# Performance work log

Hardware: AMD Instinct MI355X
Metric: run time of the kernel (lower is better)

## Reference

```python
import jax, jax.numpy as jnp
import numpy as np

NUM_TOKEN = 1024
IN_DIM = 512
OUT_DIM = 512
E = 1024          # expansion_factor * in_token_dims
S = 128
EPS = 1e-5
SQRT_S = float(np.sqrt(S))


def _rope_seq(x):
    """RoPE over axis 1 (sequence), last axis is feature dim. x: [B, L, ..., D]."""
    L = x.shape[1]
    half = x.shape[-1] // 2
    pos = jnp.arange(L, dtype=jnp.float32)
    inv_freq = 10000.0 ** (jnp.arange(half, dtype=jnp.float32) / half)
    sinusoid = pos[:, None] * inv_freq[None, :]          # [L, half]
    bshape = (1, L) + (1,) * (x.ndim - 3) + (half,)
    sin = jnp.sin(sinusoid).reshape(bshape)
    cos = jnp.cos(sinusoid).reshape(bshape)
    x1, x2 = jnp.split(x, 2, axis=-1)
    return jnp.concatenate([x1 * cos - x2 * sin, x2 * cos + x1 * sin], axis=-1)


def setup_inputs() -> dict:
    key = jax.random.key(0)
    ks = jax.random.split(key, 8)
    B = 32
    x = jax.random.normal(ks[0], (B, NUM_TOKEN, IN_DIM), jnp.float32)
    uv_w = jax.random.normal(ks[1], (2 * E + S, IN_DIM), jnp.float32) / np.sqrt(IN_DIM)
    o_w = jax.random.normal(ks[2], (OUT_DIM, E), jnp.float32) / np.sqrt(E)
    gamma = jax.random.uniform(ks[3], (2, S), jnp.float32)
    beta = jax.random.uniform(ks[4], (2, S), jnp.float32)
    w = jax.random.uniform(ks[5], (2 * NUM_TOKEN - 1,), jnp.float32)
    g = jnp.ones((1,), jnp.float32)                       # ScaleNorm gain
    res_scale = jnp.ones((IN_DIM,), jnp.float32)
    layer_scale = jnp.ones((OUT_DIM,), jnp.float32)
    return dict(x=x, uv_w=uv_w, o_w=o_w, gamma=gamma, beta=beta, w=w,
                g=g, res_scale=res_scale, layer_scale=layer_scale)


def reference(x, uv_w, o_w, gamma, beta, w, g, res_scale, layer_scale):
    B, L, D = x.shape
    # ScaleNorm
    norm = jnp.linalg.norm(x, axis=-1, keepdims=True) * (D ** -0.5)
    xn = x / jnp.maximum(norm, EPS) * g
    # shift mixing (time shift: first half channels shifted right by 1 token)
    xs, xp = jnp.split(xn, 2, axis=-1)
    xs = jnp.pad(xs, ((0, 0), (1, 0), (0, 0)))[:, :L, :]
    xn = jnp.concatenate([xs, xp], axis=-1)
    # uv projection + SiLU, then split into u, v, base
    uv = jax.nn.silu(xn @ uv_w.T)                         # [B, L, 2E+S]
    u, v, base = jnp.split(uv, [E, 2 * E], axis=-1)
    # per-head affine then RoPE
    base = base[:, :, None, :] * gamma[None, None] + beta  # [B, L, 2, S]
    base = _rope_seq(base)
    q, k = base[:, :, 0, :], base[:, :, 1, :]
    qk = jnp.einsum('bls,bms->blm', q, k)                 # [B, L, L]
    # structure-mode relative position bias: bias[i, j] = w[j - i + L - 1]
    idx = jnp.arange(L)[None, :] - jnp.arange(L)[:, None] + (L - 1)
    qk = qk + w[idx][None]
    kernel = jnp.square(jax.nn.relu(qk / SQRT_S))
    out = u * jnp.einsum('blm,bme->ble', kernel, v)       # gated quadratic attn
    out = out @ o_w.T                                     # [B, L, OUT_DIM]
    return x * res_scale + out * layer_scale
```

## Files before the change

### kernel.cpp

```cpp
#include <hip/hip_runtime.h>
#include <hip/hip_bf16.h>
#include <math.h>

typedef unsigned short u16;
typedef __bf16 bf16x8 __attribute__((ext_vector_type(8)));
typedef float f32x4 __attribute__((ext_vector_type(4)));

#define NB 32
#define LSEQ 1024
#define DIN 512
#define EDIM 1024
#define SDIM 128
#define NTOK (NB * LSEQ)
#define NUV 2176
#define CHUNK 16

#define AS1 __attribute__((address_space(1)))
#define AS3 __attribute__((address_space(3)))

__device__ __forceinline__ u16 f2bf(float f) {
  unsigned u = __builtin_bit_cast(unsigned, f);
  u += 0x7fffu + ((u >> 16) & 1u);
  return (u16)(u >> 16);
}
__device__ __forceinline__ float bf2f(u16 h) {
  unsigned u = ((unsigned)h) << 16;
  return __builtin_bit_cast(float, u);
}
__device__ __forceinline__ float fast_silu(float x) {
  float t = __builtin_amdgcn_exp2f(-1.44269504088896f * x);
  return x * __builtin_amdgcn_rcpf(1.0f + t);
}


__global__ __launch_bounds__(256) void k_f32_to_bf16(const float* __restrict__ in,
                                                     u16* __restrict__ out, int n4) {
  int i = blockIdx.x * 256 + threadIdx.x;
  if (i < n4) {
    float4 f = ((const float4*)in)[i];
    ushort4 o;
    o.x = f2bf(f.x); o.y = f2bf(f.y); o.z = f2bf(f.z); o.w = f2bf(f.w);
    ((ushort4*)out)[i] = o;
  }
}

__global__ __launch_bounds__(256) void k_normshift(const float* __restrict__ x,
                                                   const float* __restrict__ g,
                                                   u16* __restrict__ xn2) {
  int t = blockIdx.x;
  int l = t & (LSEQ - 1);
  float2 v = ((const float2*)(x + (size_t)t * DIN))[threadIdx.x];
  float ss = v.x * v.x + v.y * v.y;
  for (int o = 32; o > 0; o >>= 1) ss += __shfl_down(ss, o, 64);
  __shared__ float p[4];
  if ((threadIdx.x & 63) == 0) p[threadIdx.x >> 6] = ss;
  __syncthreads();
  float s = p[0] + p[1] + p[2] + p[3];
  float norm = sqrtf(s * (1.0f / (float)DIN));
  float inv = g[0] / fmaxf(norm, 1e-5f);
  int d = threadIdx.x * 2;
  ushort2 ob; ob.x = f2bf(v.x * inv); ob.y = f2bf(v.y * inv);
  if (d >= 256) {
    *(ushort2*)(xn2 + (size_t)t * DIN + d) = ob;
  } else {
    if (l < LSEQ - 1) *(ushort2*)(xn2 + (size_t)(t + 1) * DIN + d) = ob;
    if (l == 0) { ushort2 z = {0, 0}; *(ushort2*)(xn2 + (size_t)t * DIN + d) = z; }
  }
}

__global__ __launch_bounds__(256) void k_rope_table(float* __restrict__ sin_t,
                                                    float* __restrict__ cos_t) {
  int idx = blockIdx.x * 256 + threadIdx.x;
  int l = idx >> 6, j = idx & 63;
  double freq = pow(10000.0, (double)j / 64.0);
  float arg = (float)l * (float)freq;
  double a = (double)arg;
  sin_t[idx] = (float)sin(a);
  cos_t[idx] = (float)cos(a);
}

__global__ __launch_bounds__(256) void k_qkbuild(const u16* __restrict__ base,
                                                 const float* __restrict__ gamma,
                                                 const float* __restrict__ beta,
                                                 const float* __restrict__ sin_t,
                                                 const float* __restrict__ cos_t,
                                                 u16* __restrict__ q, u16* __restrict__ k) {
  int idx = blockIdx.x * 256 + threadIdx.x;
  int t = idx >> 6, j = idx & 63;
  int l = t & (LSEQ - 1);
  float b1 = bf2f(base[(size_t)t * SDIM + j]);
  float b2 = bf2f(base[(size_t)t * SDIM + j + 64]);
  float s = sin_t[l * 64 + j], c = cos_t[l * 64 + j];
  {
    float y1 = b1 * gamma[j] + beta[j];
    float y2 = b2 * gamma[64 + j] + beta[64 + j];
    q[(size_t)t * SDIM + j]      = f2bf(y1 * c - y2 * s);
    q[(size_t)t * SDIM + j + 64] = f2bf(y2 * c + y1 * s);
  }
  {
    float y1 = b1 * gamma[128 + j] + beta[128 + j];
    float y2 = b2 * gamma[192 + j] + beta[192 + j];
    k[(size_t)t * SDIM + j]      = f2bf(y1 * c - y2 * s);
    k[(size_t)t * SDIM + j + 64] = f2bf(y2 * c + y1 * s);
  }
}


#define GROW_A(s) (wr * 128 + (s) * 32 + wc * 8)
#define GROW_B(s) (wid * 32 + (s) * 8)

#define STG_PAIR(s, At2, Bt2, dA, dB)                                              \
  do {                                                                             \
    __builtin_amdgcn_global_load_lds(                                              \
        (AS1 unsigned int*)((At2) + (size_t)(GROW_A(s) + srow) * lda + scol),      \
        (AS3 unsigned int*)((dA) + GROW_A(s) * 64), 16, 0, 0);                     \
    __builtin_amdgcn_global_load_lds(                                              \
        (AS1 unsigned int*)((Bt2) + (size_t)(GROW_B(s) + srow) * ldb + scol),      \
        (AS3 unsigned int*)((dB) + GROW_B(s) * 64), 16, 0, 0);                     \
  } while (0)

#define RD_A(dst, cbuf, q)                                                         \
  do {                                                                             \
    _Pragma("unroll") for (int r_ = 0; r_ < 2; ++r_)                               \
    _Pragma("unroll") for (int h_ = 0; h_ < 2; ++h_)                               \
      dst[r_][h_] = *(const bf16x8*)((cbuf) + (wr * 128 + (q) * 32 + r_ * 16 + fr) * 64 + \
                                     (((h_ * 4 + kg) ^ fr7) * 8));                 \
  } while (0)

#define RD_B(cbuf)                                                                 \
  do {                                                                             \
    _Pragma("unroll") for (int n_ = 0; n_ < 4; ++n_)                               \
    _Pragma("unroll") for (int h_ = 0; h_ < 2; ++h_)                               \
      breg[n_][h_] = *(const bf16x8*)((cbuf) + (wc * 64 + n_ * 16 + fr) * 64 +     \
                                      (((h_ * 4 + kg) ^ fr7) * 8));                \
  } while (0)

#define MFMA16(s, areg)                                                            \
  do {                                                                             \
    __builtin_amdgcn_s_setprio(1);                                                 \
    _Pragma("unroll") for (int r_ = 0; r_ < 2; ++r_)                               \
    _Pragma("unroll") for (int n_ = 0; n_ < 4; ++n_)                               \
    _Pragma("unroll") for (int h_ = 0; h_ < 2; ++h_)                               \
      acc[(s) * 2 + r_][n_] = __builtin_amdgcn_mfma_f32_16x16x32_bf16(             \
          areg[r_][h_], breg[n_][h_], acc[(s) * 2 + r_][n_], 0, 0, 0);             \
    __builtin_amdgcn_s_setprio(0);                                                 \
  } while (0)

#define BAR_FENCE()                                                                \
  do { __builtin_amdgcn_s_barrier(); asm volatile("" ::: "memory"); } while (0)

#define TILE_STEP(CA, CB, OA, OB, T)                                               \
  do {                                                                             \
    const bool st_ = ((T) + 2) < nt;                                               \
    const bool more_ = ((T) + 1) < nt;                                             \
    const u16* At2_ = A + (size_t)((T) + 2) * 64;                                  \
    const u16* Bt2_ = B + (size_t)((T) + 2) * 64;                                  \
    MFMA16(0, ac);                                                                 \
    RD_A(an, CA, 1);                                                               \
    BAR_FENCE();                                                                   \
    if (st_) STG_PAIR(0, At2_, Bt2_, CA, CB);                                      \
    MFMA16(1, an);                                                                 \
    RD_A(ac, CA, 2);                                                               \
    BAR_FENCE();                                                                   \
    if (st_) STG_PAIR(1, At2_, Bt2_, CA, CB);                                      \
    MFMA16(2, ac);                                                                 \
    RD_A(an, CA, 3);                                                               \
    BAR_FENCE();                                                                   \
    if (st_) STG_PAIR(2, At2_, Bt2_, CA, CB);                                      \
    MFMA16(3, an);                                                                 \
    if (st_) asm volatile("s_waitcnt vmcnt(6)" ::: "memory");                      \
    else     asm volatile("s_waitcnt vmcnt(0)" ::: "memory");                      \
    BAR_FENCE();                                                                   \
    if (st_) STG_PAIR(3, At2_, Bt2_, CA, CB);                                      \
    if (more_) { RD_B(OB); RD_A(ac, OA, 0); }                                      \
  } while (0)

__device__ __forceinline__ void gemm256p_core(const u16* __restrict__ A, int lda,
                                              const u16* __restrict__ B, int ldb,
                                              int K, u16* smem, f32x4 (&acc)[8][4]) {
  const int tid = threadIdx.x;
  const int lane = tid & 63, wid = tid >> 6;
  const int wr = wid >> 2, wc = wid & 3;
  const int fr = lane & 15, kg = lane >> 4, fr7 = fr & 7;
  const int srow = lane >> 3;
  const int scol = ((lane & 7) ^ srow) * 8;
  u16* const A0 = smem;
  u16* const B0 = smem + 16384;
  u16* const A1 = smem + 32768;
  u16* const B1 = smem + 49152;
  const int nt = K >> 6;

#pragma unroll
  for (int s = 0; s < 4; ++s) STG_PAIR(s, A, B, A0, B0);
#pragma unroll
  for (int s = 0; s < 4; ++s) STG_PAIR(s, A + 64, B + 64, A1, B1);
  asm volatile("s_waitcnt vmcnt(8)" ::: "memory");
  BAR_FENCE();

  bf16x8 breg[4][2], ac[2][2], an[2][2];
  RD_B(B0);
  RD_A(ac, A0, 0);

  for (int tt = 0; tt < nt; tt += 2) {
    TILE_STEP(A0, B0, A1, B1, tt);
    TILE_STEP(A1, B1, A0, B0, tt + 1);
  }
}

__global__ __launch_bounds__(512, 2) void k_gemm_uv(const u16* __restrict__ xn2,
                                                    const u16* __restrict__ wbf,
                                                    u16* __restrict__ u, u16* __restrict__ vt,
                                                    u16* __restrict__ base) {
  __shared__ __align__(16) u16 smem[65536];
  f32x4 acc[8][4] = {};
  int bid = blockIdx.x;
  int xcd = bid & 7;
  int off = bid >> 3;
  int m0 = (xcd * 16 + off / 9) * 256;
  int n0 = (off % 9) * 256;
  gemm256p_core(xn2 + (size_t)m0 * DIN, DIN, wbf + (size_t)n0 * DIN, DIN, DIN, smem, acc);
  int lane = threadIdx.x & 63, wid = threadIdx.x >> 6;
  int wr = wid >> 2, wc = wid & 3;
  int cb = n0 + wc * 64 + (lane & 15);
  int rb = m0 + wr * 128 + (lane >> 4) * 4;
  if (n0 < EDIM) {
#pragma unroll
    for (int mm = 0; mm < 8; ++mm)
#pragma unroll
      for (int n = 0; n < 4; ++n) {
        int c = cb + n * 16;
#pragma unroll
        for (int j = 0; j < 4; ++j) {
          int r = rb + mm * 16 + j;
          u[(size_t)r * EDIM + c] = f2bf(fast_silu(acc[mm][n][j]));
        }
      }
  } else if (n0 < 2 * EDIM) {
    int b = m0 >> 10;
    u16* vtb = vt + (size_t)b * (EDIM * LSEQ);
#pragma unroll
    for (int mm = 0; mm < 8; ++mm) {
      int l0 = (rb + mm * 16) & (LSEQ - 1);
#pragma unroll
      for (int n = 0; n < 4; ++n) {
        int e = cb + n * 16 - EDIM;
        ushort4 o;
        o.x = f2bf(fast_silu(acc[mm][n][0]));
        o.y = f2bf(fast_silu(acc[mm][n][1]));
        o.z = f2bf(fast_silu(acc[mm][n][2]));
        o.w = f2bf(fast_silu(acc[mm][n][3]));
        *(ushort4*)(vtb + (size_t)e * LSEQ + l0) = o;
      }
    }
  } else if (wc < 2) {
#pragma unroll
    for (int mm = 0; mm < 8; ++mm)
#pragma unroll
      for (int n = 0; n < 4; ++n) {
        int c = cb + n * 16 - 2 * EDIM;
#pragma unroll
        for (int j = 0; j < 4; ++j) {
          int r = rb + mm * 16 + j;
          base[(size_t)r * SDIM + c] = f2bf(fast_silu(acc[mm][n][j]));
        }
      }
  }
}

__global__ __launch_bounds__(512, 2) void k_gemm_qk(const u16* __restrict__ q,
                                                    const u16* __restrict__ k,
                                                    const float* __restrict__ w,
                                                    u16* __restrict__ scores) {
  __shared__ __align__(16) u16 smem[65536];
  f32x4 acc[8][4] = {};
  int bid = blockIdx.x;
  int xcd = bid & 7;
  int off = bid >> 3;
  int b = xcd * 2 + (off >> 4);
  int t = off & 15;
  int m0 = (t >> 2) * 256, n0 = (t & 3) * 256;
  gemm256p_core(q + (size_t)(b * LSEQ + m0) * SDIM, SDIM,
                k + (size_t)(b * LSEQ + n0) * SDIM, SDIM,
                SDIM, smem, acc);
  int lane = threadIdx.x & 63, wid = threadIdx.x >> 6;
  int wr = wid >> 2, wc = wid & 3;
  int cb = n0 + wc * 64 + (lane & 15);
  int rb = m0 + wr * 128 + (lane >> 4) * 4;
  const float inv_sqrt_s = 0.08838834764831845f;
  u16* sc_b = scores + (size_t)b * LSEQ * LSEQ;
#pragma unroll
  for (int mm = 0; mm < 8; ++mm)
#pragma unroll
    for (int n = 0; n < 4; ++n) {
      int c = cb + n * 16;
#pragma unroll
      for (int j = 0; j < 4; ++j) {
        int r = rb + mm * 16 + j;
        float val = (acc[mm][n][j] + w[c - r + (LSEQ - 1)]) * inv_sqrt_s;
        val = fmaxf(val, 0.0f);
        sc_b[(size_t)r * LSEQ + c] = f2bf(val * val);
      }
    }
}

__global__ __launch_bounds__(512, 2) void k_gemm_pv(const u16* __restrict__ scores,
                                                    const u16* __restrict__ vt,
                                                    u16* u_io) {
  __shared__ __align__(16) u16 smem[65536];
  f32x4 acc[8][4] = {};
  int bid = blockIdx.x;
  int xcd = bid & 7;
  int off = bid >> 3;
  int b = xcd * 2 + (off >> 4);
  int t = off & 15;
  int m0 = (t >> 2) * 256, n0 = (t & 3) * 256;
  gemm256p_core(scores + (size_t)b * LSEQ * LSEQ + (size_t)m0 * LSEQ, LSEQ,
                vt + (size_t)b * LSEQ * EDIM + (size_t)n0 * LSEQ, LSEQ,
                LSEQ, smem, acc);
  int lane = threadIdx.x & 63, wid = threadIdx.x >> 6;
  int wr = wid >> 2, wc = wid & 3;
  int cb = n0 + wc * 64 + (lane & 15);
  int rb = m0 + wr * 128 + (lane >> 4) * 4;
#pragma unroll
  for (int mm = 0; mm < 8; ++mm)
#pragma unroll
    for (int n = 0; n < 4; ++n) {
      int c = cb + n * 16;
#pragma unroll
      for (int j = 0; j < 4; ++j) {
        int r = rb + mm * 16 + j;
        size_t idx = (size_t)(b * LSEQ + r) * EDIM + c;
        u_io[idx] = f2bf(acc[mm][n][j] * bf2f(u_io[idx]));
      }
    }
}

__global__ __launch_bounds__(512, 2) void k_gemm_out(const u16* __restrict__ attn,
                                                     const u16* __restrict__ owbf,
                                                     const float* __restrict__ x,
                                                     const float* __restrict__ res_scale,
                                                     const float* __restrict__ layer_scale,
                                                     float* __restrict__ out) {
  __shared__ __align__(16) u16 smem[65536];
  f32x4 acc[8][4] = {};
  int bid = blockIdx.x;
  int xcd = bid & 7;
  int off = bid >> 3;
  int m0 = (xcd * 16 + (off >> 1)) * 256;
  int n0 = (off & 1) * 256;
  gemm256p_core(attn + (size_t)m0 * EDIM, EDIM, owbf + (size_t)n0 * EDIM, EDIM,
                EDIM, smem, acc);
  int lane = threadIdx.x & 63, wid = threadIdx.x >> 6;
  int wr = wid >> 2, wc = wid & 3;
  int cb = n0 + wc * 64 + (lane & 15);
  int rb = m0 + wr * 128 + (lane >> 4) * 4;
#pragma unroll
  for (int mm = 0; mm < 8; ++mm)
#pragma unroll
    for (int n = 0; n < 4; ++n) {
      int c = cb + n * 16;
#pragma unroll
      for (int j = 0; j < 4; ++j) {
        int r = rb + mm * 16 + j;
        out[(size_t)r * DIN + c] =
            x[(size_t)r * DIN + c] * res_scale[c] + acc[mm][n][j] * layer_scale[c];
      }
    }
}


extern "C" void kernel_launch(void* const* d_in, const int* in_sizes, int n_in,
                              void* d_out, int out_size, void* d_ws, size_t ws_size,
                              hipStream_t stream) {
  const float* x          = (const float*)d_in[0];
  const float* uv_w       = (const float*)d_in[1];
  const float* o_w        = (const float*)d_in[2];
  const float* gamma      = (const float*)d_in[3];
  const float* beta       = (const float*)d_in[4];
  const float* w          = (const float*)d_in[5];
  const float* g          = (const float*)d_in[6];
  const float* res_scale  = (const float*)d_in[7];
  const float* layer_scale= (const float*)d_in[8];
  float* out = (float*)d_out;

  char* ws = (char*)d_ws;
  u16* xn2    = (u16*)(ws + 0);
  u16* q      = (u16*)(ws + 0);
  u16* k      = (u16*)(ws + 8388608);
  u16* scores = (u16*)(ws + 16777216);
  u16* base   = (u16*)(ws + 33554432);
  u16* u_io   = (u16*)(ws + 50331648);
  u16* vt     = (u16*)(ws + 117440512);
  u16* uvw_bf = (u16*)(ws + 184549376);
  u16* ow_bf  = (u16*)(ws + 186908672);
  float* sin_t = (float*)(ws + 187957248);
  float* cos_t = (float*)(ws + 188219392);

  k_f32_to_bf16<<<dim3((NUV * DIN / 4 + 255) / 256), 256, 0, stream>>>(uv_w, uvw_bf, NUV * DIN / 4);
  k_f32_to_bf16<<<dim3((DIN * EDIM / 4 + 255) / 256), 256, 0, stream>>>(o_w, ow_bf, DIN * EDIM / 4);
  k_rope_table<<<dim3(LSEQ * 64 / 256), 256, 0, stream>>>(sin_t, cos_t);
  k_normshift<<<dim3(NTOK), 256, 0, stream>>>(x, g, xn2);

  k_gemm_uv<<<dim3(1152), 512, 0, stream>>>(xn2, uvw_bf, u_io, vt, base);

  k_qkbuild<<<dim3(NTOK * 64 / 256), 256, 0, stream>>>(base, gamma, beta, sin_t, cos_t, q, k);

  for (int ch = 0; ch < NB / CHUNK; ++ch) {
    size_t tok0 = (size_t)ch * CHUNK * LSEQ;
    k_gemm_qk<<<dim3(256), 512, 0, stream>>>(q + tok0 * SDIM, k + tok0 * SDIM, w, scores);
    k_gemm_pv<<<dim3(256), 512, 0, stream>>>(scores, vt + tok0 * EDIM, u_io + tok0 * EDIM);
  }

  k_gemm_out<<<dim3(256), 512, 0, stream>>>(u_io, ow_bf, x, res_scale, layer_scale, out);
}
```

Measured before the change: 316.8 us.

## Restructure GEMM main loop into barrier-bracketed phases with staggered LDS staging

Rewrites the double-buffered 256x256 GEMM mainloop into four phases per K-tile. Each phase reads its A fragment from LDS, issues a reshuffled set of global-to-LDS loads, waits on lgkmcnt, and runs its MFMAs between two barriers. The last A sub-tile of the next buffer is now staged in the following iteration, and B staging is spread over phases, to balance memory traffic against compute. The cost is twice as many barriers and less register double-buffering of A fragments, which may expose LDS read latency.

After: 336.6 us. 1.06x slower.

```diff
diff --git a/kernel.cpp b/kernel.cpp
--- a/kernel.cpp
+++ b/kernel.cpp
@@ -109,15 +109,14 @@
 #define GROW_A(s) (wr * 128 + (s) * 32 + wc * 8)
 #define GROW_B(s) (wid * 32 + (s) * 8)
 
-#define STG_PAIR(s, At2, Bt2, dA, dB)                                              \
-  do {                                                                             \
-    __builtin_amdgcn_global_load_lds(                                              \
-        (AS1 unsigned int*)((At2) + (size_t)(GROW_A(s) + srow) * lda + scol),      \
-        (AS3 unsigned int*)((dA) + GROW_A(s) * 64), 16, 0, 0);                     \
-    __builtin_amdgcn_global_load_lds(                                              \
-        (AS1 unsigned int*)((Bt2) + (size_t)(GROW_B(s) + srow) * ldb + scol),      \
-        (AS3 unsigned int*)((dB) + GROW_B(s) * 64), 16, 0, 0);                     \
-  } while (0)
+#define STG_A(s, Asrc, dA)                                                         \
+  __builtin_amdgcn_global_load_lds(                                               \
+      (AS1 unsigned int*)((Asrc) + (size_t)(GROW_A(s) + srow) * lda + scol),       \
+      (AS3 unsigned int*)((dA) + GROW_A(s) * 64), 16, 0, 0)
+#define STG_B(s, Bsrc, dB)                                                         \
+  __builtin_amdgcn_global_load_lds(                                               \
+      (AS1 unsigned int*)((Bsrc) + (size_t)(GROW_B(s) + srow) * ldb + scol),       \
+      (AS3 unsigned int*)((dB) + GROW_B(s) * 64), 16, 0, 0)
 
 #define RD_A(dst, cbuf, q)                                                         \
   do {                                                                             \
@@ -149,30 +148,40 @@
 #define BAR_FENCE()                                                                \
   do { __builtin_amdgcn_s_barrier(); asm volatile("" ::: "memory"); } while (0)
 
-#define TILE_STEP(CA, CB, OA, OB, T)                                               \
+#define PH_BAR_MFMA(q)                                                             \
   do {                                                                             \
-    const bool st_ = ((T) + 2) < nt;                                               \
-    const bool more_ = ((T) + 1) < nt;                                             \
+    BAR_FENCE();                                                                   \
+    asm volatile("s_waitcnt lgkmcnt(0)" ::: "memory");                             \
+    __builtin_amdgcn_sched_barrier(0);                                             \
+    MFMA16(q, aq);                                                                 \
+    BAR_FENCE();                                                                   \
+  } while (0)
+
+#define TILE8(CA, CB, OA, T)                                                       \
+  do {                                                                             \
+    const u16* At1_ = A + (size_t)((T) + 1) * 64;                                  \
     const u16* At2_ = A + (size_t)((T) + 2) * 64;                                  \
     const u16* Bt2_ = B + (size_t)((T) + 2) * 64;                                  \
-    MFMA16(0, ac);                                                                 \
-    RD_A(an, CA, 1);                                                               \
-    BAR_FENCE();                                                                   \
-    if (st_) STG_PAIR(0, At2_, Bt2_, CA, CB);                                      \
-    MFMA16(1, an);                                                                 \
-    RD_A(ac, CA, 2);                                                               \
-    BAR_FENCE();                                                                   \
-    if (st_) STG_PAIR(1, At2_, Bt2_, CA, CB);                                      \
-    MFMA16(2, ac);                                                                 \
-    RD_A(an, CA, 3);                                                               \
-    BAR_FENCE();                                                                   \
-    if (st_) STG_PAIR(2, At2_, Bt2_, CA, CB);                                      \
-    MFMA16(3, an);                                                                 \
-    if (st_) asm volatile("s_waitcnt vmcnt(6)" ::: "memory");                      \
-    else     asm volatile("s_waitcnt vmcnt(0)" ::: "memory");                      \
-    BAR_FENCE();                                                                   \
-    if (st_) STG_PAIR(3, At2_, Bt2_, CA, CB);                                      \
-    if (more_) { RD_B(OB); RD_A(ac, OA, 0); }                                      \
+    const bool s1_ = ((T) + 1) < nt;                                               \
+    const bool s2_ = ((T) + 2) < nt;                                               \
+                                                                      \
+    RD_B(CB); RD_A(aq, CA, 0);                                                     \
+    if (s1_) STG_A(3, At1_, OA);                                                   \
+    asm volatile("s_waitcnt lgkmcnt(8)" ::: "memory");                             \
+    PH_BAR_MFMA(0);                                                                \
+                                                                      \
+    RD_A(aq, CA, 1);                                                               \
+    if (s2_) { STG_A(0, At2_, CA); STG_B(0, Bt2_, CB); STG_B(1, Bt2_, CB); }       \
+    PH_BAR_MFMA(1);                                                                \
+                                                                      \
+    RD_A(aq, CA, 2);                                                               \
+    if (s2_) { STG_A(1, At2_, CA); STG_B(2, Bt2_, CB); STG_B(3, Bt2_, CB); }       \
+    PH_BAR_MFMA(2);                                                                \
+                                     \
+    RD_A(aq, CA, 3);                                                               \
+    if (s2_) { STG_A(2, At2_, CA); asm volatile("s_waitcnt vmcnt(7)" ::: "memory"); } \
+    else     { asm volatile("s_waitcnt vmcnt(0)" ::: "memory"); }                  \
+    PH_BAR_MFMA(3);                                                                \
   } while (0)
 
 __device__ __forceinline__ void gemm256p_core(const u16* __restrict__ A, int lda,
@@ -190,20 +199,19 @@
   u16* const B1 = smem + 49152;
   const int nt = K >> 6;
 
-#pragma unroll
-  for (int s = 0; s < 4; ++s) STG_PAIR(s, A, B, A0, B0);
-#pragma unroll
-  for (int s = 0; s < 4; ++s) STG_PAIR(s, A + 64, B + 64, A1, B1);
-  asm volatile("s_waitcnt vmcnt(8)" ::: "memory");
+  STG_A(0, A, A0); STG_A(1, A, A0); STG_A(2, A, A0); STG_A(3, A, A0);
+  STG_B(0, B, B0); STG_B(1, B, B0); STG_B(2, B, B0); STG_B(3, B, B0);
+  STG_A(0, A + 64, A1); STG_A(1, A + 64, A1); STG_A(2, A + 64, A1);
+  STG_B(0, B + 64, B1); STG_B(1, B + 64, B1); STG_B(2, B + 64, B1); STG_B(3, B + 64, B1);
+  asm volatile("s_waitcnt vmcnt(7)" ::: "memory");
+  __builtin_amdgcn_sched_barrier(0);
   BAR_FENCE();
 
-  bf16x8 breg[4][2], ac[2][2], an[2][2];
-  RD_B(B0);
-  RD_A(ac, A0, 0);
+  bf16x8 breg[4][2], aq[2][2];
 
   for (int tt = 0; tt < nt; tt += 2) {
-    TILE_STEP(A0, B0, A1, B1, tt);
-    TILE_STEP(A1, B1, A0, B0, tt + 1);
+    TILE8(A0, B0, A1, tt);
+    TILE8(A1, B1, A0, tt + 1);
   }
 }
 
```
